# Performance work log

Hardware: AMD Instinct MI355X
Metric: run time of the kernel (lower is better)

The kernel has to match this reference:

```python
import jax, jax.numpy as jnp
import numpy as np

B, L, NIN, H, D = 512, 100, 3, 256, 10
WIN = 5  # hardcoded attention window in the original loop (out[:, i-5:i, :])


def _gru_layer(x, Wih, Whh, bih, bhh):
    # x: [B, L, in]; PyTorch GRU gate math, gates ordered (r, z, n)
    xw = jnp.einsum('bli,gi->blg', x, Wih) + bih  # [B, L, 3H]
    h0 = jnp.zeros((x.shape[0], Whh.shape[1]), x.dtype)

    def step(h, xt):
        gh = h @ Whh.T + bhh
        xr, xz, xn = jnp.split(xt, 3, axis=-1)
        hr, hz, hn = jnp.split(gh, 3, axis=-1)
        r = jax.nn.sigmoid(xr + hr)
        z = jax.nn.sigmoid(xz + hz)
        n = jnp.tanh(xn + r * hn)
        h_new = (1.0 - z) * n + z * h
        return h_new, h_new

    _, ys = jax.lax.scan(step, h0, jnp.swapaxes(xw, 0, 1))
    return jnp.swapaxes(ys, 0, 1)  # [B, L, H]


def _gru2(x, Wih0, Whh0, bih0, bhh0, Wih1, Whh1, bih1, bhh1):
    h1 = _gru_layer(x, Wih0, Whh0, bih0, bhh0)
    return _gru_layer(h1, Wih1, Whh1, bih1, bhh1)


def _branch(out, attn_w, fc_W, fc_b):
    # score(i, k) = [q_i ; e_{i-5+k}] . attn_w  (linear on concat, no bias)
    q = out @ attn_w[:H]   # [B, L] query part
    e = out @ attn_w[H:]   # [B, L] key part
    M = L - WIN
    win = jnp.stack([out[:, k:k + M] for k in range(WIN)], axis=2)  # [B, M, 5, H]
    ewin = jnp.stack([e[:, k:k + M] for k in range(WIN)], axis=2)    # [B, M, 5]
    scores = q[:, WIN:, None] + ewin
    a = jax.nn.softmax(scores, axis=-1)
    c = jnp.einsum('blw,blwh->blh', a, win)                          # [B, M, H]
    fused = jnp.concatenate([c, out[:, WIN:]], axis=-1) @ fc_W.T + fc_b
    # timesteps 0..4 pass through unchanged
    return jnp.concatenate([out[:, :WIN], fused], axis=1)            # [B, L, H]


def setup_inputs() -> dict:
    key = jax.random.key(0)
    ks = iter(jax.random.split(key, 32))
    s = 0.08

    def p(shape):
        return s * jax.random.normal(next(ks), shape, dtype=jnp.float32)

    inp = {'received': jax.random.normal(next(ks), (B, L, NIN), dtype=jnp.float32)}
    for r in ('r1', 'r2'):
        inp[f'{r}_Wih0'] = p((3 * H, NIN))
        inp[f'{r}_Whh0'] = p((3 * H, H))
        inp[f'{r}_bih0'] = p((3 * H,))
        inp[f'{r}_bhh0'] = p((3 * H,))
        inp[f'{r}_Wih1'] = p((3 * H, H))
        inp[f'{r}_Whh1'] = p((3 * H, H))
        inp[f'{r}_bih1'] = p((3 * H,))
        inp[f'{r}_bhh1'] = p((3 * H,))
    inp['attn_w'] = p((2 * H,))
    inp['fc_W'] = p((H, 2 * H))
    inp['fc_b'] = p((H,))
    inp['out_W'] = p((1, 2 * H))
    inp['out_b'] = p((1,))
    return inp


def reference(received,
              r1_Wih0, r1_Whh0, r1_bih0, r1_bhh0, r1_Wih1, r1_Whh1, r1_bih1, r1_bhh1,
              r2_Wih0, r2_Whh0, r2_bih0, r2_bhh0, r2_Wih1, r2_Whh1, r2_bih1, r2_bhh1,
              attn_w, fc_W, fc_b, out_W, out_b):
    out1 = _gru2(received, r1_Wih0, r1_Whh0, r1_bih0, r1_bhh0,
                 r1_Wih1, r1_Whh1, r1_bih1, r1_bhh1)
    out2 = _gru2(received, r2_Wih0, r2_Whh0, r2_bih0, r2_bhh0,
                 r2_Wih1, r2_Whh1, r2_bih1, r2_bhh1)
    rnn_out1 = _branch(out1, attn_w, fc_W, fc_b)
    rnn_out2 = _branch(out2, attn_w, fc_W, fc_b)
    # delay alignment: rt_d[i] = rnn_out2[min(i+D, L-1)]
    idx = jnp.minimum(jnp.arange(L) + D, L - 1)
    rt_d = rnn_out2[:, idx]
    rnn_out = jnp.concatenate([rnn_out1, rt_d], axis=-1)  # [B, L, 2H]
    dec = rnn_out @ out_W.T + out_b                       # dec_act = 'linear'
    return jax.nn.sigmoid(dec)                            # [B, L, 1]
```

## Files before the change

kernel.cpp:

```cpp
#include <hip/hip_runtime.h>
#include <hip/hip_bf16.h>

#define BQ 512
#define LQ 100
#define HQ 256
#define GQ 768
#define WINQ 5
#define MQ 95
#define HPAD 264

typedef __hip_bfloat16 bf16;
typedef unsigned short u16;
typedef __attribute__((ext_vector_type(8))) short short8;
typedef __attribute__((ext_vector_type(4))) float f32x4;

__device__ __forceinline__ float bf2f(bf16 v) { return __bfloat162float(v); }
__device__ __forceinline__ bf16 f2bf(float v) { return __float2bfloat16(v); }
__device__ __forceinline__ u16 f2bfb(float v) { return __builtin_bit_cast(u16, __float2bfloat16(v)); }
__device__ __forceinline__ float bfb2f(u16 u) {
  unsigned int x = ((unsigned int)u) << 16;
  return __builtin_bit_cast(float, x);
}
__device__ __forceinline__ float rcpf(float x) { return __builtin_amdgcn_rcpf(x); }
__device__ __forceinline__ float sigmf(float x) { return rcpf(1.0f + __expf(-x)); }
__device__ __forceinline__ float tanh_fast(float x) {
  float ax = fabsf(x);
  float e = __expf(-2.0f * ax);
  float t = (1.0f - e) * rcpf(1.0f + e);
  return copysignf(t, x);
}
__device__ __forceinline__ short8 ld8(const u16* p) { return *(const short8*)p; }
__device__ __forceinline__ void st8nt(u16* p, short8 v) {
  __builtin_nontemporal_store(v, (short8*)p);
}
__device__ __forceinline__ f32x4 mfma16(short8 a, short8 b, f32x4 c) {
  return __builtin_amdgcn_mfma_f32_16x16x32_bf16(a, b, c, 0, 0, 0);
}
__device__ __forceinline__ void gl_lds16(const u16* g, u16* l) {
  __builtin_amdgcn_global_load_lds(
      (const __attribute__((address_space(1))) unsigned int*)g,
      (__attribute__((address_space(3))) unsigned int*)l, 16, 0, 0);
}
__device__ __forceinline__ int xwl_idx(int col, int m) {
  int ch = col >> 3;
  return ch * 128 + ((m ^ (ch & 15)) << 3) + (col & 7);
}

__global__ __launch_bounds__(256) void cvt7_kernel(
    const float* __restrict__ s0, const float* __restrict__ s1,
    const float* __restrict__ s2, const float* __restrict__ s3,
    const float* __restrict__ s4, const float* __restrict__ s5,
    const float* __restrict__ s6,
    u16* __restrict__ d0, u16* __restrict__ d1, u16* __restrict__ d2,
    u16* __restrict__ d3, u16* __restrict__ d4, u16* __restrict__ d5,
    u16* __restrict__ d6) {
  const int seg = blockIdx.y;
  const float* s; u16* d; int n4;
  switch (seg) {
    case 0: s = s0; d = d0; n4 = GQ * HQ / 4; break;
    case 1: s = s1; d = d1; n4 = GQ * HQ / 4; break;
    case 2: s = s2; d = d2; n4 = GQ * HQ / 4; break;
    case 3: s = s3; d = d3; n4 = GQ * HQ / 4; break;
    case 4: s = s4; d = d4; n4 = GQ * HQ / 4; break;
    case 5: s = s5; d = d5; n4 = GQ * HQ / 4; break;
    default: s = s6; d = d6; n4 = HQ * 512 / 4; break;
  }
  int i = blockIdx.x * 256 + threadIdx.x;
  if (i < n4) {
    float4 v = reinterpret_cast<const float4*>(s)[i];
    ushort4 o;
    o.x = f2bfb(v.x); o.y = f2bfb(v.y); o.z = f2bfb(v.z); o.w = f2bfb(v.w);
    reinterpret_cast<ushort4*>(d)[i] = o;
  }
}

__global__ __launch_bounds__(256) void xw0_kernel(
    const float* __restrict__ x,
    const float* __restrict__ WihA, const float* __restrict__ bihA,
    const float* __restrict__ WihB, const float* __restrict__ bihB,
    u16* __restrict__ xw) {
  const int r = blockIdx.y;
  const float* Wih = r ? WihB : WihA;
  const float* bih = r ? bihB : bihA;
  const int row0 = blockIdx.x * 16;
  u16* o = xw + (size_t)r * BQ * LQ * GQ;
  const int g = threadIdx.x;

  __shared__ float xs[16][3];
  if (threadIdx.x < 48) {
    int m = threadIdx.x / 3, i = threadIdx.x - m * 3;
    xs[m][i] = x[(size_t)(row0 + m) * 3 + i];
  }
  float wv[3][3], bv[3];
  #pragma unroll
  for (int s = 0; s < 3; ++s) {
    int gg = g + s * 256;
    wv[s][0] = Wih[gg * 3]; wv[s][1] = Wih[gg * 3 + 1]; wv[s][2] = Wih[gg * 3 + 2];
    bv[s] = bih[gg];
  }
  __syncthreads();
  for (int m = 0; m < 16; ++m) {
    const float x0 = xs[m][0], x1 = xs[m][1], x2 = xs[m][2];
    u16* orow = o + (size_t)(row0 + m) * GQ;
    #pragma unroll
    for (int s = 0; s < 3; ++s)
      orow[s * 256 + g] = f2bfb(fmaf(x0, wv[s][0], fmaf(x1, wv[s][1], fmaf(x2, wv[s][2], bv[s]))));
  }
}

__global__ __launch_bounds__(256) void xw1_gemm_kernel(
    const u16* __restrict__ o0A, const u16* __restrict__ o0B,
    const u16* __restrict__ wihA, const u16* __restrict__ wihB,
    const float* __restrict__ bihA, const float* __restrict__ bihB,
    u16* __restrict__ xw) {
  const int r = blockIdx.y;
  const u16* A = r ? o0B : o0A;
  const u16* Wih = r ? wihB : wihA;
  const float* bih = r ? bihB : bihA;
  u16* out = xw + (size_t)r * BQ * LQ * GQ;
  const int row0 = blockIdx.x * 64;
  const int tid = threadIdx.x;
  const int w = tid >> 6, lane = tid & 63, l15 = lane & 15, quad = lane >> 4;

  __shared__ u16 a_lds[64][HPAD];
  for (int g = tid; g < 64 * 32; g += 256) {
    int rr = g >> 5, c8 = (g & 31) * 8;
    *(short8*)&a_lds[rr][c8] = ld8(&A[(size_t)(row0 + rr) * HQ + c8]);
  }
  __syncthreads();

  for (int nt = 0; nt < 12; ++nt) {
    const int n0 = w * 192 + nt * 16;
    const u16* bp = Wih + (size_t)(n0 + l15) * HQ + quad * 8;
    short8 b[8];
    #pragma unroll
    for (int kt = 0; kt < 8; ++kt) b[kt] = ld8(bp + kt * 32);
    const float bias = bih[n0 + l15];
    #pragma unroll
    for (int mt = 0; mt < 4; ++mt) {
      f32x4 acc = {bias, bias, bias, bias};
      #pragma unroll
      for (int kt = 0; kt < 8; ++kt) {
        short8 a = ld8(&a_lds[mt * 16 + l15][kt * 32 + quad * 8]);
        acc = mfma16(a, b[kt], acc);
      }
      #pragma unroll
      for (int reg = 0; reg < 4; ++reg) {
        int row = row0 + mt * 16 + quad * 4 + reg;
        out[(size_t)row * GQ + n0 + l15] = f2bfb(acc[reg]);
      }
    }
  }
}

__global__ __launch_bounds__(512, 2) void scan_mfma_kernel(
    const u16* __restrict__ xwA, const u16* __restrict__ xwB,
    const u16* __restrict__ whhA, const u16* __restrict__ whhB,
    const float* __restrict__ bhhA, const float* __restrict__ bhhB,
    u16* __restrict__ outA, u16* __restrict__ outB) {
  const int r = blockIdx.y;
  const u16* xw = r ? xwB : xwA;
  const u16* whh = r ? whhB : whhA;
  const float* bhh = r ? bhhB : bhhA;
  u16* out = r ? outB : outA;
  const int b0 = blockIdx.x * 16;
  const int tid = threadIdx.x;
  const int w = tid >> 6, lane = tid & 63, l15 = lane & 15, quad = lane >> 4;
  const int jbase = w * 32;

  __shared__ u16 h_lds[2][16][HPAD];
  __shared__ u16 xwl[2][16 * GQ];
  __shared__ u16 wc[8][10][512];

  for (int i = tid; i < 16 * HPAD; i += 512)
    h_lds[0][i / HPAD][i % HPAD] = 0;

  #pragma unroll
  for (int i = 0; i < 5; ++i) {
    const u16* bp = whh + (size_t)((i >> 1) * HQ + jbase + (i & 1) * 16 + l15) * HQ + quad * 8;
    #pragma unroll
    for (int kt = 0; kt < 2; ++kt)
      *(short8*)&wc[w][i * 2 + kt][lane * 8] = ld8(bp + kt * 32);
  }
  float bh[6];
  #pragma unroll
  for (int i = 0; i < 6; ++i)
    bh[i] = bhh[(i >> 1) * HQ + jbase + (i & 1) * 16 + l15];

  const u16* gsrc[3];
  int ldsoff[3];
  #pragma unroll
  for (int k = 0; k < 3; ++k) {
    int c0k = (w * 3 + k) * 64;
    int s = c0k + lane;
    int ch = s >> 4;
    int m = (s & 15) ^ (ch & 15);
    gsrc[k] = xw + (size_t)(b0 + m) * LQ * GQ + ch * 8;
    ldsoff[k] = c0k * 8;
  }
  const int om = tid >> 5, oc = (tid & 31) * 8;

  #pragma unroll
  for (int k = 0; k < 3; ++k) gl_lds16(gsrc[k], &xwl[0][ldsoff[k]]);

  __syncthreads();

  for (int t = 0; t < LQ; ++t) {
    const int rb = t & 1, wb = rb ^ 1;

    const int tn = (t + 1 < LQ) ? t + 1 : t;
    #pragma unroll
    for (int k = 0; k < 3; ++k)
      gl_lds16(gsrc[k] + (size_t)tn * GQ, &xwl[wb][ldsoff[k]]);

    short8 a[8];
    #pragma unroll
    for (int kt = 0; kt < 8; ++kt)
      a[kt] = ld8(&h_lds[rb][l15][kt * 32 + quad * 8]);

    if (t > 0) {
      short8 h0 = ld8(&h_lds[rb][om][oc]);
      st8nt(&out[((size_t)(b0 + om) * LQ + (t - 1)) * HQ + oc], h0);
    }

    #pragma unroll
    for (int jt = 0; jt < 2; ++jt) {
      f32x4 accr = {bh[jt], bh[jt], bh[jt], bh[jt]};
      f32x4 accz = {bh[2 + jt], bh[2 + jt], bh[2 + jt], bh[2 + jt]};
      f32x4 accn = {bh[4 + jt], bh[4 + jt], bh[4 + jt], bh[4 + jt]};
      const u16* bp0 = whh + (size_t)(jbase + jt * 16 + l15) * HQ + quad * 8;
      const u16* bp1 = bp0 + (size_t)HQ * HQ;
      const u16* bp2 = bp1 + (size_t)HQ * HQ;
      #pragma unroll
      for (int kt = 0; kt < 8; ++kt) {
        short8 br, bz, bn;
        if (kt < 2) {
          br = ld8(&wc[w][(0 * 2 + jt) * 2 + kt][lane * 8]);
          bz = ld8(&wc[w][(1 * 2 + jt) * 2 + kt][lane * 8]);
          bn = (jt == 0) ? ld8(&wc[w][(2 * 2 + jt) * 2 + kt][lane * 8])
                         : ld8(bp2 + kt * 32);
        } else {
          br = ld8(bp0 + kt * 32);
          bz = ld8(bp1 + kt * 32);
          bn = ld8(bp2 + kt * 32);
        }
        accr = mfma16(a[kt], br, accr);
        accz = mfma16(a[kt], bz, accz);
        accn = mfma16(a[kt], bn, accn);
      }
      const int j = jbase + jt * 16 + l15;
      #pragma unroll
      for (int reg = 0; reg < 4; ++reg) {
        const int m = quad * 4 + reg;
        const float xr = bfb2f(xwl[rb][xwl_idx(j, m)]);
        const float xz = bfb2f(xwl[rb][xwl_idx(HQ + j, m)]);
        const float xn = bfb2f(xwl[rb][xwl_idx(2 * HQ + j, m)]);
        const float hold = bfb2f(h_lds[rb][m][j]);
        const float rg = sigmf(accr[reg] + xr);
        const float zg = sigmf(accz[reg] + xz);
        const float ng = tanh_fast(fmaf(rg, accn[reg], xn));
        const float hn = fmaf(zg, hold - ng, ng);
        h_lds[wb][m][j] = f2bfb(hn);
      }
    }
    __syncthreads();
  }

  {
    short8 h0 = ld8(&h_lds[0][om][oc]);
    st8nt(&out[((size_t)(b0 + om) * LQ + (LQ - 1)) * HQ + oc], h0);
  }
}

__global__ __launch_bounds__(256) void attn_fused_kernel(
    const u16* __restrict__ out1, const u16* __restrict__ out2,
    const float* __restrict__ attn_w,
    u16* __restrict__ c1, u16* __restrict__ c2) {
  const int b = blockIdx.x;
  const int br = blockIdx.y;
  const u16* out = br ? out2 : out1;
  u16* cb = br ? c2 : c1;
  const int tid = threadIdx.x;
  const int w = tid >> 6, lane = tid & 63;

  __shared__ u16 ol[LQ][HPAD];
  __shared__ float qv[LQ], ev[LQ];

  for (int idx = tid; idx < LQ * 32; idx += 256) {
    int row = idx >> 5, c8 = (idx & 31) * 8;
    *(short8*)&ol[row][c8] = ld8(&out[((size_t)b * LQ + row) * HQ + c8]);
  }
  __syncthreads();

  float aq[4], ae[4];
  #pragma unroll
  for (int jj = 0; jj < 4; ++jj) {
    aq[jj] = attn_w[lane + 64 * jj];
    ae[jj] = attn_w[HQ + lane + 64 * jj];
  }
  for (int l = w; l < LQ; l += 4) {
    float sq = 0.f, se = 0.f;
    #pragma unroll
    for (int jj = 0; jj < 4; ++jj) {
      float v = bfb2f(ol[l][lane + 64 * jj]);
      sq = fmaf(v, aq[jj], sq);
      se = fmaf(v, ae[jj], se);
    }
    #pragma unroll
    for (int o = 32; o > 0; o >>= 1) { sq += __shfl_down(sq, o); se += __shfl_down(se, o); }
    if (lane == 0) { qv[l] = sq; ev[l] = se; }
  }
  __syncthreads();

  for (int m = 0; m < MQ; ++m) {
    const float qq = qv[m + WINQ];
    float s[WINQ];
    float mx = -1e30f;
    #pragma unroll
    for (int k = 0; k < WINQ; ++k) { s[k] = qq + ev[m + k]; mx = fmaxf(mx, s[k]); }
    float sum = 0.f;
    #pragma unroll
    for (int k = 0; k < WINQ; ++k) { s[k] = __expf(s[k] - mx); sum += s[k]; }
    const float inv = rcpf(sum);
    float accv = 0.f;
    #pragma unroll
    for (int k = 0; k < WINQ; ++k)
      accv = fmaf(s[k], bfb2f(ol[m + k][tid]), accv);
    cb[((size_t)b * MQ + m) * HQ + tid] = f2bfb(accv * inv);
  }
}

__global__ __launch_bounds__(256) void fc_mfma_kernel(
    const u16* __restrict__ c1, const u16* __restrict__ c2,
    const u16* __restrict__ o1, const u16* __restrict__ o2,
    const u16* __restrict__ fcw, const float* __restrict__ fcb,
    u16* __restrict__ f1, u16* __restrict__ f2) {
  const int br = blockIdx.y;
  const u16* cb = br ? c2 : c1;
  const u16* ob = br ? o2 : o1;
  u16* fo = br ? f2 : f1;
  const int i0 = blockIdx.x * 64;
  const int tid = threadIdx.x;
  const int w = tid >> 6, lane = tid & 63, l15 = lane & 15, quad = lane >> 4;

  __shared__ u16 a_lds[64][520];
  for (int g = tid; g < 64 * 64; g += 256) {
    int rr = g >> 6, c8 = (g & 63) * 8;
    int gi = i0 + rr;
    int bb = gi / MQ, mm = gi - bb * MQ;
    const u16* src = (c8 < HQ) ? &cb[(size_t)gi * HQ + c8]
                               : &ob[((size_t)bb * LQ + mm + WINQ) * HQ + (c8 - HQ)];
    *(short8*)&a_lds[rr][c8] = ld8(src);
  }
  __syncthreads();

  for (int nt = 0; nt < 4; ++nt) {
    const int n0 = w * 64 + nt * 16;
    const u16* bp = fcw + (size_t)(n0 + l15) * 512 + quad * 8;
    short8 b[16];
    #pragma unroll
    for (int kt = 0; kt < 16; ++kt) b[kt] = ld8(bp + kt * 32);
    const float bias = fcb[n0 + l15];
    #pragma unroll
    for (int mt = 0; mt < 4; ++mt) {
      f32x4 acc = {bias, bias, bias, bias};
      #pragma unroll
      for (int kt = 0; kt < 16; ++kt) {
        short8 a = ld8(&a_lds[mt * 16 + l15][kt * 32 + quad * 8]);
        acc = mfma16(a, b[kt], acc);
      }
      #pragma unroll
      for (int reg = 0; reg < 4; ++reg)
        fo[(size_t)(i0 + mt * 16 + quad * 4 + reg) * HQ + n0 + l15] = f2bfb(acc[reg]);
    }
  }
}

__global__ __launch_bounds__(256) void final_kernel(
    const bf16* __restrict__ out1,
    const bf16* __restrict__ f1, const bf16* __restrict__ f2,
    const float* __restrict__ outW, const float* __restrict__ outb,
    float* __restrict__ dout) {
  const int wid = blockIdx.x * 4 + (threadIdx.x >> 6);
  const int lane = threadIdx.x & 63;
  const int b = wid / LQ, l = wid - b * LQ;
  const bf16* s1 = (l < WINQ) ? (out1 + ((size_t)b * LQ + l) * HQ)
                              : (f1 + ((size_t)b * MQ + (l - WINQ)) * HQ);
  int l2 = l + 10;
  if (l2 > LQ - 1) l2 = LQ - 1;
  const bf16* s2 = f2 + ((size_t)b * MQ + (l2 - WINQ)) * HQ;
  float s = 0.0f;
  #pragma unroll
  for (int jj = 0; jj < 4; ++jj) {
    int h = lane + jj * 64;
    s = fmaf(bf2f(s1[h]), outW[h], s);
    s = fmaf(bf2f(s2[h]), outW[HQ + h], s);
  }
  #pragma unroll
  for (int o = 32; o > 0; o >>= 1) s += __shfl_down(s, o);
  if (lane == 0) dout[wid] = sigmf(s + outb[0]);
}

extern "C" void kernel_launch(void* const* d_in, const int* in_sizes, int n_in,
                              void* d_out, int out_size, void* d_ws, size_t ws_size,
                              hipStream_t stream) {
  const float* x       = (const float*)d_in[0];
  const float* r1_Wih0 = (const float*)d_in[1];
  const float* r1_Whh0 = (const float*)d_in[2];
  const float* r1_bih0 = (const float*)d_in[3];
  const float* r1_bhh0 = (const float*)d_in[4];
  const float* r1_Wih1 = (const float*)d_in[5];
  const float* r1_Whh1 = (const float*)d_in[6];
  const float* r1_bih1 = (const float*)d_in[7];
  const float* r1_bhh1 = (const float*)d_in[8];
  const float* r2_Wih0 = (const float*)d_in[9];
  const float* r2_Whh0 = (const float*)d_in[10];
  const float* r2_bih0 = (const float*)d_in[11];
  const float* r2_bhh0 = (const float*)d_in[12];
  const float* r2_Wih1 = (const float*)d_in[13];
  const float* r2_Whh1 = (const float*)d_in[14];
  const float* r2_bih1 = (const float*)d_in[15];
  const float* r2_bhh1 = (const float*)d_in[16];
  const float* attn_w  = (const float*)d_in[17];
  const float* fc_W    = (const float*)d_in[18];
  const float* fc_b    = (const float*)d_in[19];
  const float* out_W   = (const float*)d_in[20];
  const float* out_b   = (const float*)d_in[21];

  char* p = (char*)d_ws;
  auto carve = [&](size_t bytes) {
    char* r = p;
    p += ((bytes + 255) / 256) * 256;
    return r;
  };
  const size_t WSZ = (size_t)GQ * HQ;
  const size_t XWR = (size_t)BQ * LQ * GQ;
  const size_t SEQ = (size_t)BQ * LQ * HQ;
  const size_t FSEQ = (size_t)BQ * MQ * HQ;

  u16* whh0A = (u16*)carve(WSZ * 2);
  u16* whh0B = (u16*)carve(WSZ * 2);
  u16* whh1A = (u16*)carve(WSZ * 2);
  u16* whh1B = (u16*)carve(WSZ * 2);
  u16* wih1A = (u16*)carve(WSZ * 2);
  u16* wih1B = (u16*)carve(WSZ * 2);
  u16* fcwbf = (u16*)carve((size_t)HQ * 512 * 2);
  u16* xwbuf = (u16*)carve(XWR * 2 * 2);
  u16* obuf  = (u16*)carve(SEQ * 2 * 2);

  u16* xwA = xwbuf;
  u16* xwB = xwbuf + XWR;
  u16* oA  = obuf;
  u16* oB  = obuf + SEQ;
  u16* c1 = xwbuf;
  u16* c2 = c1 + FSEQ;
  u16* f1 = c2 + FSEQ;
  u16* f2 = f1 + FSEQ;

  cvt7_kernel<<<dim3((WSZ / 4 + 255) / 256, 7), 256, 0, stream>>>(
      r1_Whh0, r2_Whh0, r1_Whh1, r2_Whh1, r1_Wih1, r2_Wih1, fc_W,
      whh0A, whh0B, whh1A, whh1B, wih1A, wih1B, fcwbf);

  xw0_kernel<<<dim3(BQ * LQ / 16, 2), 256, 0, stream>>>(
      x, r1_Wih0, r1_bih0, r2_Wih0, r2_bih0, xwbuf);
  scan_mfma_kernel<<<dim3(BQ / 16, 2), 512, 0, stream>>>(
      xwA, xwB, whh0A, whh0B, r1_bhh0, r2_bhh0, oA, oB);
  xw1_gemm_kernel<<<dim3(BQ * LQ / 64, 2), 256, 0, stream>>>(
      oA, oB, wih1A, wih1B, r1_bih1, r2_bih1, xwbuf);
  scan_mfma_kernel<<<dim3(BQ / 16, 2), 512, 0, stream>>>(
      xwA, xwB, whh1A, whh1B, r1_bhh1, r2_bhh1, oA, oB);

  attn_fused_kernel<<<dim3(BQ, 2), 256, 0, stream>>>(oA, oB, attn_w, c1, c2);
  fc_mfma_kernel<<<dim3((BQ * MQ) / 64, 2), 256, 0, stream>>>(c1, c2, oA, oB, fcwbf, fc_b, f1, f2);
  final_kernel<<<(BQ * LQ) / 4, 256, 0, stream>>>(
      (const bf16*)oA, (const bf16*)f1, (const bf16*)f2, out_W, out_b, (float*)d_out);
}
```

Measured before the change: 996.0 us.

## Fuse weight conversion with xw0, fuse attention with FC, enlarge GEMM tiles

Merges the bf16 weight conversion into the layer-0 input-projection kernel, which now writes 16-byte nontemporal stores. Fuses the sliding-window attention with the FC MFMA GEMM per batch row so the context tensor stays in LDS instead of going through global memory. Doubles the xw1 GEMM row tile to 128 and caches one more Whh fragment in LDS in the scan kernel. These changes remove launches and intermediate traffic, but the fused attention kernel uses about 150KB of LDS per block, which limits occupancy, and the FC tile is padded from 95 to 96 rows.

```diff
diff --git a/kernel.cpp b/kernel.cpp
--- a/kernel.cpp
+++ b/kernel.cpp
@@ -15,7 +15,6 @@
 typedef __attribute__((ext_vector_type(4))) float f32x4;
 
 __device__ __forceinline__ float bf2f(bf16 v) { return __bfloat162float(v); }
-__device__ __forceinline__ bf16 f2bf(float v) { return __float2bfloat16(v); }
 __device__ __forceinline__ u16 f2bfb(float v) { return __builtin_bit_cast(u16, __float2bfloat16(v)); }
 __device__ __forceinline__ float bfb2f(u16 u) {
   unsigned int x = ((unsigned int)u) << 16;
@@ -46,7 +45,11 @@
   return ch * 128 + ((m ^ (ch & 15)) << 3) + (col & 7);
 }
 
-__global__ __launch_bounds__(256) void cvt7_kernel(
+__global__ __launch_bounds__(256) void cvt_xw0_kernel(
+    const float* __restrict__ x,
+    const float* __restrict__ Wih0A, const float* __restrict__ bih0A,
+    const float* __restrict__ Wih0B, const float* __restrict__ bih0B,
+    u16* __restrict__ xw,
     const float* __restrict__ s0, const float* __restrict__ s1,
     const float* __restrict__ s2, const float* __restrict__ s3,
     const float* __restrict__ s4, const float* __restrict__ s5,
@@ -54,57 +57,51 @@
     u16* __restrict__ d0, u16* __restrict__ d1, u16* __restrict__ d2,
     u16* __restrict__ d3, u16* __restrict__ d4, u16* __restrict__ d5,
     u16* __restrict__ d6) {
-  const int seg = blockIdx.y;
-  const float* s; u16* d; int n4;
-  switch (seg) {
-    case 0: s = s0; d = d0; n4 = GQ * HQ / 4; break;
-    case 1: s = s1; d = d1; n4 = GQ * HQ / 4; break;
-    case 2: s = s2; d = d2; n4 = GQ * HQ / 4; break;
-    case 3: s = s3; d = d3; n4 = GQ * HQ / 4; break;
-    case 4: s = s4; d = d4; n4 = GQ * HQ / 4; break;
-    case 5: s = s5; d = d5; n4 = GQ * HQ / 4; break;
-    default: s = s6; d = d6; n4 = HQ * 512 / 4; break;
-  }
-  int i = blockIdx.x * 256 + threadIdx.x;
-  if (i < n4) {
-    float4 v = reinterpret_cast<const float4*>(s)[i];
-    ushort4 o;
-    o.x = f2bfb(v.x); o.y = f2bfb(v.y); o.z = f2bfb(v.z); o.w = f2bfb(v.w);
-    reinterpret_cast<ushort4*>(d)[i] = o;
-  }
-}
-
-__global__ __launch_bounds__(256) void xw0_kernel(
-    const float* __restrict__ x,
-    const float* __restrict__ WihA, const float* __restrict__ bihA,
-    const float* __restrict__ WihB, const float* __restrict__ bihB,
-    u16* __restrict__ xw) {
-  const int r = blockIdx.y;
-  const float* Wih = r ? WihB : WihA;
-  const float* bih = r ? bihB : bihA;
+  const int y = blockIdx.y;
+  const int tid = threadIdx.x;
+  if (y >= 2) {
+    const int seg = y - 2;
+    const float* s; u16* d; int n4;
+    switch (seg) {
+      case 0: s = s0; d = d0; n4 = GQ * HQ / 4; break;
+      case 1: s = s1; d = d1; n4 = GQ * HQ / 4; break;
+      case 2: s = s2; d = d2; n4 = GQ * HQ / 4; break;
+      case 3: s = s3; d = d3; n4 = GQ * HQ / 4; break;
+      case 4: s = s4; d = d4; n4 = GQ * HQ / 4; break;
+      case 5: s = s5; d = d5; n4 = GQ * HQ / 4; break;
+      default: s = s6; d = d6; n4 = HQ * 512 / 4; break;
+    }
+    int i = blockIdx.x * 256 + tid;
+    if (i < n4) {
+      float4 v = reinterpret_cast<const float4*>(s)[i];
+      ushort4 o;
+      o.x = f2bfb(v.x); o.y = f2bfb(v.y); o.z = f2bfb(v.z); o.w = f2bfb(v.w);
+      reinterpret_cast<ushort4*>(d)[i] = o;
+    }
+    return;
+  }
+  const float* Wih = y ? Wih0B : Wih0A;
+  const float* bih = y ? bih0B : bih0A;
   const int row0 = blockIdx.x * 16;
-  u16* o = xw + (size_t)r * BQ * LQ * GQ;
-  const int g = threadIdx.x;
+  u16* o = xw + (size_t)y * BQ * LQ * GQ;
 
   __shared__ float xs[16][3];
-  if (threadIdx.x < 48) {
-    int m = threadIdx.x / 3, i = threadIdx.x - m * 3;
+  if (tid < 48) {
+    int m = tid / 3, i = tid - m * 3;
     xs[m][i] = x[(size_t)(row0 + m) * 3 + i];
   }
-  float wv[3][3], bv[3];
-  #pragma unroll
-  for (int s = 0; s < 3; ++s) {
-    int gg = g + s * 256;
-    wv[s][0] = Wih[gg * 3]; wv[s][1] = Wih[gg * 3 + 1]; wv[s][2] = Wih[gg * 3 + 2];
-    bv[s] = bih[gg];
-  }
-  __syncthreads();
-  for (int m = 0; m < 16; ++m) {
+  __syncthreads();
+  for (int idx = tid; idx < 16 * 96; idx += 256) {
+    const int m = idx / 96, ch = idx - m * 96;
     const float x0 = xs[m][0], x1 = xs[m][1], x2 = xs[m][2];
-    u16* orow = o + (size_t)(row0 + m) * GQ;
-    #pragma unroll
-    for (int s = 0; s < 3; ++s)
-      orow[s * 256 + g] = f2bfb(fmaf(x0, wv[s][0], fmaf(x1, wv[s][1], fmaf(x2, wv[s][2], bv[s]))));
+    short8 ov;
+    #pragma unroll
+    for (int e = 0; e < 8; ++e) {
+      const int g = ch * 8 + e;
+      float v = fmaf(x0, Wih[g * 3], fmaf(x1, Wih[g * 3 + 1], fmaf(x2, Wih[g * 3 + 2], bih[g])));
+      ov[e] = (short)f2bfb(v);
+    }
+    st8nt(o + (size_t)(row0 + m) * GQ + ch * 8, ov);
   }
 }
 
@@ -118,12 +115,12 @@
   const u16* Wih = r ? wihB : wihA;
   const float* bih = r ? bihB : bihA;
   u16* out = xw + (size_t)r * BQ * LQ * GQ;
-  const int row0 = blockIdx.x * 64;
+  const int row0 = blockIdx.x * 128;
   const int tid = threadIdx.x;
   const int w = tid >> 6, lane = tid & 63, l15 = lane & 15, quad = lane >> 4;
 
-  __shared__ u16 a_lds[64][HPAD];
-  for (int g = tid; g < 64 * 32; g += 256) {
+  __shared__ u16 a_lds[128][HPAD];
+  for (int g = tid; g < 128 * 32; g += 256) {
     int rr = g >> 5, c8 = (g & 31) * 8;
     *(short8*)&a_lds[rr][c8] = ld8(&A[(size_t)(row0 + rr) * HQ + c8]);
   }
@@ -137,7 +134,7 @@
     for (int kt = 0; kt < 8; ++kt) b[kt] = ld8(bp + kt * 32);
     const float bias = bih[n0 + l15];
     #pragma unroll
-    for (int mt = 0; mt < 4; ++mt) {
+    for (int mt = 0; mt < 8; ++mt) {
       f32x4 acc = {bias, bias, bias, bias};
       #pragma unroll
       for (int kt = 0; kt < 8; ++kt) {
@@ -170,17 +167,20 @@
 
   __shared__ u16 h_lds[2][16][HPAD];
   __shared__ u16 xwl[2][16 * GQ];
-  __shared__ u16 wc[8][10][512];
+  __shared__ u16 wc[8][11][512];
 
   for (int i = tid; i < 16 * HPAD; i += 512)
     h_lds[0][i / HPAD][i % HPAD] = 0;
 
   #pragma unroll
-  for (int i = 0; i < 5; ++i) {
+  for (int i = 0; i < 6; ++i) {
     const u16* bp = whh + (size_t)((i >> 1) * HQ + jbase + (i & 1) * 16 + l15) * HQ + quad * 8;
     #pragma unroll
-    for (int kt = 0; kt < 2; ++kt)
-      *(short8*)&wc[w][i * 2 + kt][lane * 8] = ld8(bp + kt * 32);
+    for (int kt = 0; kt < 2; ++kt) {
+      const int f = i * 2 + kt;
+      if (f < 11)
+        *(short8*)&wc[w][f][lane * 8] = ld8(bp + kt * 32);
+    }
   }
   float bh[6];
   #pragma unroll
@@ -234,16 +234,10 @@
       #pragma unroll
       for (int kt = 0; kt < 8; ++kt) {
         short8 br, bz, bn;
-        if (kt < 2) {
-          br = ld8(&wc[w][(0 * 2 + jt) * 2 + kt][lane * 8]);
-          bz = ld8(&wc[w][(1 * 2 + jt) * 2 + kt][lane * 8]);
-          bn = (jt == 0) ? ld8(&wc[w][(2 * 2 + jt) * 2 + kt][lane * 8])
-                         : ld8(bp2 + kt * 32);
-        } else {
-          br = ld8(bp0 + kt * 32);
-          bz = ld8(bp1 + kt * 32);
-          bn = ld8(bp2 + kt * 32);
-        }
+        const int i0t = 0 * 2 + jt, i1t = 1 * 2 + jt, i2t = 2 * 2 + jt;
+        br = (kt < 2 && i0t * 2 + kt < 11) ? ld8(&wc[w][i0t * 2 + kt][lane * 8]) : ld8(bp0 + kt * 32);
+        bz = (kt < 2 && i1t * 2 + kt < 11) ? ld8(&wc[w][i1t * 2 + kt][lane * 8]) : ld8(bp1 + kt * 32);
+        bn = (kt < 2 && i2t * 2 + kt < 11) ? ld8(&wc[w][i2t * 2 + kt][lane * 8]) : ld8(bp2 + kt * 32);
         accr = mfma16(a[kt], br, accr);
         accz = mfma16(a[kt], bz, accz);
         accn = mfma16(a[kt], bn, accn);
@@ -272,21 +266,23 @@
   }
 }
 
-__global__ __launch_bounds__(256) void attn_fused_kernel(
+__global__ __launch_bounds__(512) void attnfc_kernel(
     const u16* __restrict__ out1, const u16* __restrict__ out2,
     const float* __restrict__ attn_w,
-    u16* __restrict__ c1, u16* __restrict__ c2) {
+    const u16* __restrict__ fcw, const float* __restrict__ fcb,
+    u16* __restrict__ f1, u16* __restrict__ f2) {
   const int b = blockIdx.x;
   const int br = blockIdx.y;
   const u16* out = br ? out2 : out1;
-  u16* cb = br ? c2 : c1;
+  u16* fo = br ? f2 : f1;
   const int tid = threadIdx.x;
-  const int w = tid >> 6, lane = tid & 63;
+  const int w = tid >> 6, lane = tid & 63, l15 = lane & 15, quad = lane >> 4;
 
   __shared__ u16 ol[LQ][HPAD];
+  __shared__ u16 al[96][520];
   __shared__ float qv[LQ], ev[LQ];
 
-  for (int idx = tid; idx < LQ * 32; idx += 256) {
+  for (int idx = tid; idx < LQ * 32; idx += 512) {
     int row = idx >> 5, c8 = (idx & 31) * 8;
     *(short8*)&ol[row][c8] = ld8(&out[((size_t)b * LQ + row) * HQ + c8]);
   }
@@ -298,7 +294,7 @@
     aq[jj] = attn_w[lane + 64 * jj];
     ae[jj] = attn_w[HQ + lane + 64 * jj];
   }
-  for (int l = w; l < LQ; l += 4) {
+  for (int l = w; l < LQ; l += 8) {
     float sq = 0.f, se = 0.f;
     #pragma unroll
     for (int jj = 0; jj < 4; ++jj) {
@@ -312,66 +308,52 @@
   }
   __syncthreads();
 
-  for (int m = 0; m < MQ; ++m) {
-    const float qq = qv[m + WINQ];
-    float s[WINQ];
-    float mx = -1e30f;
-    #pragma unroll
-    for (int k = 0; k < WINQ; ++k) { s[k] = qq + ev[m + k]; mx = fmaxf(mx, s[k]); }
-    float sum = 0.f;
-    #pragma unroll
-    for (int k = 0; k < WINQ; ++k) { s[k] = __expf(s[k] - mx); sum += s[k]; }
-    const float inv = rcpf(sum);
-    float accv = 0.f;
-    #pragma unroll
-    for (int k = 0; k < WINQ; ++k)
-      accv = fmaf(s[k], bfb2f(ol[m + k][tid]), accv);
-    cb[((size_t)b * MQ + m) * HQ + tid] = f2bfb(accv * inv);
-  }
-}
-
-__global__ __launch_bounds__(256) void fc_mfma_kernel(
-    const u16* __restrict__ c1, const u16* __restrict__ c2,
-    const u16* __restrict__ o1, const u16* __restrict__ o2,
-    const u16* __restrict__ fcw, const float* __restrict__ fcb,
-    u16* __restrict__ f1, u16* __restrict__ f2) {
-  const int br = blockIdx.y;
-  const u16* cb = br ? c2 : c1;
-  const u16* ob = br ? o2 : o1;
-  u16* fo = br ? f2 : f1;
-  const int i0 = blockIdx.x * 64;
-  const int tid = threadIdx.x;
-  const int w = tid >> 6, lane = tid & 63, l15 = lane & 15, quad = lane >> 4;
-
-  __shared__ u16 a_lds[64][520];
-  for (int g = tid; g < 64 * 64; g += 256) {
-    int rr = g >> 6, c8 = (g & 63) * 8;
-    int gi = i0 + rr;
-    int bb = gi / MQ, mm = gi - bb * MQ;
-    const u16* src = (c8 < HQ) ? &cb[(size_t)gi * HQ + c8]
-                               : &ob[((size_t)bb * LQ + mm + WINQ) * HQ + (c8 - HQ)];
-    *(short8*)&a_lds[rr][c8] = ld8(src);
-  }
-  __syncthreads();
-
-  for (int nt = 0; nt < 4; ++nt) {
-    const int n0 = w * 64 + nt * 16;
+  {
+    const int half = tid >> 8, col = tid & 255;
+    const int mlo = half * 48, mhi = half ? 95 : 48;
+    for (int m = mlo; m < mhi; ++m) {
+      const float qq = qv[m + WINQ];
+      float s[WINQ];
+      float mx = -1e30f;
+      #pragma unroll
+      for (int k = 0; k < WINQ; ++k) { s[k] = qq + ev[m + k]; mx = fmaxf(mx, s[k]); }
+      float sum = 0.f;
+      #pragma unroll
+      for (int k = 0; k < WINQ; ++k) { s[k] = __expf(s[k] - mx); sum += s[k]; }
+      const float inv = rcpf(sum);
+      float accv = 0.f;
+      #pragma unroll
+      for (int k = 0; k < WINQ; ++k)
+        accv = fmaf(s[k], bfb2f(ol[m + k][col]), accv);
+      al[m][col] = f2bfb(accv * inv);
+      al[m][HQ + col] = ol[m + WINQ][col];
+    }
+    if (half == 0) { al[95][col] = 0; al[95][HQ + col] = 0; }
+  }
+  __syncthreads();
+
+  #pragma unroll
+  for (int nt = 0; nt < 2; ++nt) {
+    const int n0 = (w * 2 + nt) * 16;
     const u16* bp = fcw + (size_t)(n0 + l15) * 512 + quad * 8;
-    short8 b[16];
-    #pragma unroll
-    for (int kt = 0; kt < 16; ++kt) b[kt] = ld8(bp + kt * 32);
+    short8 bfr[16];
+    #pragma unroll
+    for (int kt = 0; kt < 16; ++kt) bfr[kt] = ld8(bp + kt * 32);
     const float bias = fcb[n0 + l15];
     #pragma unroll
-    for (int mt = 0; mt < 4; ++mt) {
+    for (int mt = 0; mt < 6; ++mt) {
       f32x4 acc = {bias, bias, bias, bias};
       #pragma unroll
       for (int kt = 0; kt < 16; ++kt) {
-        short8 a = ld8(&a_lds[mt * 16 + l15][kt * 32 + quad * 8]);
-        acc = mfma16(a, b[kt], acc);
-      }
-      #pragma unroll
-      for (int reg = 0; reg < 4; ++reg)
-        fo[(size_t)(i0 + mt * 16 + quad * 4 + reg) * HQ + n0 + l15] = f2bfb(acc[reg]);
+        short8 a = ld8(&al[mt * 16 + l15][kt * 32 + quad * 8]);
+        acc = mfma16(a, bfr[kt], acc);
+      }
+      #pragma unroll
+      for (int reg = 0; reg < 4; ++reg) {
+        const int row = mt * 16 + quad * 4 + reg;
+        if (row < MQ)
+          fo[((size_t)b * MQ + row) * HQ + n0 + l15] = f2bfb(acc[reg]);
+      }
     }
   }
 }
@@ -452,26 +434,22 @@
   u16* xwB = xwbuf + XWR;
   u16* oA  = obuf;
   u16* oB  = obuf + SEQ;
-  u16* c1 = xwbuf;
-  u16* c2 = c1 + FSEQ;
-  u16* f1 = c2 + FSEQ;
+  u16* f1 = xwbuf;
   u16* f2 = f1 + FSEQ;
 
-  cvt7_kernel<<<dim3((WSZ / 4 + 255) / 256, 7), 256, 0, stream>>>(
+  cvt_xw0_kernel<<<dim3(BQ * LQ / 16, 9), 256, 0, stream>>>(
+      x, r1_Wih0, r1_bih0, r2_Wih0, r2_bih0, xwbuf,
       r1_Whh0, r2_Whh0, r1_Whh1, r2_Whh1, r1_Wih1, r2_Wih1, fc_W,
       whh0A, whh0B, whh1A, whh1B, wih1A, wih1B, fcwbf);
 
-  xw0_kernel<<<dim3(BQ * LQ / 16, 2), 256, 0, stream>>>(
-      x, r1_Wih0, r1_bih0, r2_Wih0, r2_bih0, xwbuf);
   scan_mfma_kernel<<<dim3(BQ / 16, 2), 512, 0, stream>>>(
       xwA, xwB, whh0A, whh0B, r1_bhh0, r2_bhh0, oA, oB);
-  xw1_gemm_kernel<<<dim3(BQ * LQ / 64, 2), 256, 0, stream>>>(
+  xw1_gemm_kernel<<<dim3(BQ * LQ / 128, 2), 256, 0, stream>>>(
       oA, oB, wih1A, wih1B, r1_bih1, r2_bih1, xwbuf);
   scan_mfma_kernel<<<dim3(BQ / 16, 2), 512, 0, stream>>>(
       xwA, xwB, whh1A, whh1B, r1_bhh1, r2_bhh1, oA, oB);
 
-  attn_fused_kernel<<<dim3(BQ, 2), 256, 0, stream>>>(oA, oB, attn_w, c1, c2);
-  fc_mfma_kernel<<<dim3((BQ * MQ) / 64, 2), 256, 0, stream>>>(c1, c2, oA, oB, fcwbf, fc_b, f1, f2);
+  attnfc_kernel<<<dim3(BQ, 2), 512, 0, stream>>>(oA, oB, attn_w, fcwbf, fc_b, f1, f2);
   final_kernel<<<(BQ * LQ) / 4, 256, 0, stream>>>(
       (const bf16*)oA, (const bf16*)f1, (const bf16*)f2, out_W, out_b, (float*)d_out);
 }
```

Result: slower. 1.156 ms (+16.1%).
